# Kernel tuning notes

Hardware: AMD Instinct MI355X
Metric: run time of the kernel (lower is better)

Reference implementation:

```python
import jax, jax.numpy as jnp
from jax import lax
import numpy as np

WIN = 11
SIGMA = 1.5
PAD = WIN // 2
C1 = 0.01 ** 2
C2 = 0.03 ** 2


def _gauss1d():
    x = jnp.arange(WIN, dtype=jnp.float32) - (WIN // 2)
    k = jnp.exp(-(x ** 2) / (2.0 * SIGMA ** 2))
    return k / k.sum()


def _blur3d(x, k1d):
    # Separable 3D gaussian blur (mathematically identical to the outer-product
    # 3D kernel used by the torch module, since kernel3d = k1d (x) k1d (x) k1d).
    # x: [B, 1, D, H, W]
    dn = ('NCDHW', 'OIDHW', 'NCDHW')
    x = lax.conv_general_dilated(x, k1d.reshape(1, 1, WIN, 1, 1), (1, 1, 1),
                                 [(PAD, PAD), (0, 0), (0, 0)], dimension_numbers=dn)
    x = lax.conv_general_dilated(x, k1d.reshape(1, 1, 1, WIN, 1), (1, 1, 1),
                                 [(0, 0), (PAD, PAD), (0, 0)], dimension_numbers=dn)
    x = lax.conv_general_dilated(x, k1d.reshape(1, 1, 1, 1, WIN), (1, 1, 1),
                                 [(0, 0), (0, 0), (PAD, PAD)], dimension_numbers=dn)
    return x


def setup_inputs() -> dict:
    key = jax.random.key(0)
    k1, k2 = jax.random.split(key)
    shape = (2, 1, 192, 192, 192)
    img1 = jax.random.uniform(k1, shape, dtype=jnp.float32)
    img2 = jax.random.uniform(k2, shape, dtype=jnp.float32)
    return {"img1": img1, "img2": img2}


def reference(img1, img2):
    k1d = _gauss1d().astype(img1.dtype)
    mu1 = _blur3d(img1, k1d)
    mu2 = _blur3d(img2, k1d)
    mu1_sq = mu1 * mu1
    mu2_sq = mu2 * mu2
    mu1mu2 = mu1 * mu2
    sigma1 = _blur3d(img1 * img1, k1d) - mu1_sq
    sigma2 = _blur3d(img2 * img2, k1d) - mu2_sq
    sigma12 = _blur3d(img1 * img2, k1d) - mu1mu2
    num = (2.0 * mu1mu2 + C1) * (2.0 * sigma12 + C2)
    den = (mu1_sq + mu2_sq + C1) * (sigma1 + sigma2 + C2)
    ssim_map = num / den
    return ssim_map.mean()  # size_average=True
```

## Files before the change

kernel.cpp:

```cpp
#include <hip/hip_runtime.h>

#define NB 2
#define DD 192
#define HH 192
#define WW 192
#define HWSZ (HH * WW)
#define C1F 0.0001f
#define C2F 0.0009f

#define TH 16
#define TW 32
#define CHUNK 24
#define TSTEPS (CHUNK + 10)
#define NCH (DD / CHUNK)
#define NTH (HH / TH)
#define NTW (WW / TW)
#define NBLK (NB * NCH * NTH * NTW)

#define SROWS (TH + 10)
#define SCOLS 42
#define SQ 43
#define TQ 36
#define NSTG (SROWS * SCOLS)
#define NWT (SROWS * (TW / 4))

#define KWLIST { 0.00102838f, 0.00759876f, 0.03600077f, 0.10936071f, 0.21300556f, \
                 0.26601172f, 0.21300556f, 0.10936071f, 0.03600077f, 0.00759876f, 0.00102838f }

__device__ __forceinline__ float ssim_val(float mu1, float mu2, float A, float Bm) {
  const float mu1sq = mu1 * mu1, mu2sq = mu2 * mu2, mu12 = mu1 * mu2;
  const float num = (2.f * mu12 + C1F) * (0.5f * (A - Bm) - 2.f * mu12 + C2F);
  const float den = (mu1sq + mu2sq + C1F) * (0.5f * (A + Bm) - mu1sq - mu2sq + C2F);
  return num * __builtin_amdgcn_rcpf(den);
}

__global__ __launch_bounds__(256) void ssim_fused(
    const float* __restrict__ x, const float* __restrict__ y,
    float* __restrict__ partials) {
  const float KW[11] = KWLIST;

  int bid = blockIdx.x;
  const int tw = bid % NTW; bid /= NTW;
  const int th = bid % NTH; bid /= NTH;
  const int c  = bid % NCH; bid /= NCH;
  const int b  = bid;
  const int h0 = th * TH, w0 = tw * TW, c0 = c * CHUNK;

  __shared__ float4 s4[SROWS][SQ];
  __shared__ float4 t4[SROWS][TQ];

  const int tid = threadIdx.x;
  const int cl  = tid & 31;
  const int rg  = tid >> 5;
  const int r0  = 2 * rg;
  const int clp2 = (cl & ~3) | (((cl & 3) + (cl >> 2)) & 3);

  int  sIdx[5], sOff[5];
  bool sOk[5];
#pragma unroll
  for (int k = 0; k < 5; ++k) {
    const int q = tid + 256 * k;
    const bool act = (q < NSTG);
    const int row = q / SCOLS, col = q % SCOLS;
    const int gh = h0 - 5 + row, gw = w0 - 5 + col;
    sOk[k]  = act && (unsigned)gh < (unsigned)HH && (unsigned)gw < (unsigned)WW;
    sIdx[k] = row * SQ + col;
    sOff[k] = gh * WW + gw;
  }
  const bool wAct = (tid < NWT);
  const int  wr = tid >> 3;
  const int  wq = tid & 7;
  const int  tBase = wr * TQ + 4 * wq;
  const int  st0 = tBase + ((0 + wq) & 3);
  const int  st1 = tBase + ((1 + wq) & 3);
  const int  st2 = tBase + ((2 + wq) & 3);
  const int  st3 = tBase + ((3 + wq) & 3);

  {
    const float4 z = make_float4(0.f, 0.f, 0.f, 0.f);
    for (int q = tid; q < SROWS * SQ; q += 256) (&s4[0][0])[q] = z;
  }
  __syncthreads();

  const float* xb = x + (size_t)b * DD * HWSZ;
  const float* yb = y + (size_t)b * DD * HWSZ;

  float pend0[4][11], pend1[4][11];
#pragma unroll
  for (int f = 0; f < 4; ++f)
#pragma unroll
    for (int i = 0; i < 11; ++i) { pend0[f][i] = 0.f; pend1[f][i] = 0.f; }

  float px[5], py[5];
#pragma unroll
  for (int k = 0; k < 5; ++k) { px[k] = 0.f; py[k] = 0.f; }

  if (c0 >= 5) {
    const float* xs = xb + (size_t)(c0 - 5) * HWSZ;
    const float* ys = yb + (size_t)(c0 - 5) * HWSZ;
#pragma unroll
    for (int k = 0; k < 5; ++k)
      if (sOk[k]) { px[k] = xs[sOff[k]]; py[k] = ys[sOff[k]]; }
  }

  float lsum = 0.f;
  int p = 0;

  for (int t = 0; t < TSTEPS; ++t) {
    const int d = c0 - 5 + t;
    const bool dv = (d >= 0) && (d < DD);

    if (dv) {
#pragma unroll
      for (int k = 0; k < 5; ++k)
        if (sOk[k]) {
          const float xx = px[k], yy = py[k];
          const float sm = xx + yy, df = xx - yy;
          (&s4[0][0])[sIdx[k]] = make_float4(xx, yy, sm * sm, df * df);
        }
    }
    {
      const int dn = d + 1;
      if ((t + 1) < TSTEPS && dn >= 0 && dn < DD) {
        const float* xs = xb + (size_t)dn * HWSZ;
        const float* ys = yb + (size_t)dn * HWSZ;
#pragma unroll
        for (int k = 0; k < 5; ++k)
          if (sOk[k]) { px[k] = xs[sOff[k]]; py[k] = ys[sOff[k]]; }
      }
    }

    float4 B0 = make_float4(0.f, 0.f, 0.f, 0.f);
    float4 B1 = B0;

    if (dv) {
      __syncthreads();
      if (wAct) {
        const float4* srow = &s4[wr][0];
        float4 a0 = make_float4(0.f, 0.f, 0.f, 0.f), a1 = a0, a2 = a0, a3 = a0;
#pragma unroll
        for (int u = 0; u < 14; ++u) {
          const float4 v = srow[4 * wq + u];
          if (u <= 10)           { const float k = KW[u];     a0.x += k*v.x; a0.y += k*v.y; a0.z += k*v.z; a0.w += k*v.w; }
          if (u >= 1 && u <= 11) { const float k = KW[u - 1]; a1.x += k*v.x; a1.y += k*v.y; a1.z += k*v.z; a1.w += k*v.w; }
          if (u >= 2 && u <= 12) { const float k = KW[u - 2]; a2.x += k*v.x; a2.y += k*v.y; a2.z += k*v.z; a2.w += k*v.w; }
          if (u >= 3)            { const float k = KW[u - 3]; a3.x += k*v.x; a3.y += k*v.y; a3.z += k*v.z; a3.w += k*v.w; }
        }
        float4* tb = &t4[0][0];
        tb[st0] = a0; tb[st1] = a1; tb[st2] = a2; tb[st3] = a3;
      }
      __syncthreads();

#pragma unroll
      for (int u = 0; u < 12; ++u) {
        const float4 v = t4[r0 + u][clp2];
        if (u <= 10) { const float k = KW[u];     B0.x += k*v.x; B0.y += k*v.y; B0.z += k*v.z; B0.w += k*v.w; }
        if (u >= 1)  { const float k = KW[u - 1]; B1.x += k*v.x; B1.y += k*v.y; B1.z += k*v.z; B1.w += k*v.w; }
      }
    }

#define RING_CASE(P)                                                        \
    case P: {                                                               \
      if (dv) {                                                             \
        _Pragma("unroll")                                                   \
        for (int kk = 0; kk < 11; ++kk) {                                   \
          const int   sl = (P + 1 + kk) % 11;                               \
          const float wg = KW[kk];                                          \
          pend0[0][sl] += wg * B0.x; pend0[1][sl] += wg * B0.y;             \
          pend0[2][sl] += wg * B0.z; pend0[3][sl] += wg * B0.w;             \
          pend1[0][sl] += wg * B1.x; pend1[1][sl] += wg * B1.y;             \
          pend1[2][sl] += wg * B1.z; pend1[3][sl] += wg * B1.w;             \
        }                                                                   \
      }                                                                     \
      const int sc = (P + 1) % 11;                                          \
      if (t >= 10) {                                                        \
        lsum += ssim_val(pend0[0][sc], pend0[1][sc], pend0[2][sc], pend0[3][sc]); \
        lsum += ssim_val(pend1[0][sc], pend1[1][sc], pend1[2][sc], pend1[3][sc]); \
      }                                                                     \
      pend0[0][sc] = 0.f; pend0[1][sc] = 0.f;                               \
      pend0[2][sc] = 0.f; pend0[3][sc] = 0.f;                               \
      pend1[0][sc] = 0.f; pend1[1][sc] = 0.f;                               \
      pend1[2][sc] = 0.f; pend1[3][sc] = 0.f;                               \
    } break;

    switch (p) {
      RING_CASE(0) RING_CASE(1) RING_CASE(2) RING_CASE(3) RING_CASE(4)
      RING_CASE(5) RING_CASE(6) RING_CASE(7) RING_CASE(8) RING_CASE(9)
      RING_CASE(10)
    }
#undef RING_CASE
    p = (p + 1 == 11) ? 0 : p + 1;
  }

  for (int off = 32; off > 0; off >>= 1) lsum += __shfl_down(lsum, off, 64);
  __shared__ float wsum[4];
  if ((tid & 63) == 0) wsum[tid >> 6] = lsum;
  __syncthreads();
  if (tid == 0) partials[blockIdx.x] = wsum[0] + wsum[1] + wsum[2] + wsum[3];
}

__global__ __launch_bounds__(256) void ssim_reduce(
    const float* __restrict__ partials, float* __restrict__ out) {
  __shared__ double sd[256];
  double a = 0.0;
  for (int i = threadIdx.x; i < NBLK; i += 256) a += (double)partials[i];
  sd[threadIdx.x] = a;
  __syncthreads();
  for (int s = 128; s > 0; s >>= 1) {
    if ((int)threadIdx.x < s) sd[threadIdx.x] += sd[threadIdx.x + s];
    __syncthreads();
  }
  if (threadIdx.x == 0) {
    out[0] = (float)(sd[0] / (double)((size_t)NB * DD * HH * WW));
  }
}

extern "C" void kernel_launch(void* const* d_in, const int* in_sizes, int n_in,
                              void* d_out, int out_size, void* d_ws, size_t ws_size,
                              hipStream_t stream) {
  const float* img1 = (const float*)d_in[0];
  const float* img2 = (const float*)d_in[1];
  float* out = (float*)d_out;
  float* partials = (float*)d_ws;

  ssim_fused<<<NBLK, 256, 0, stream>>>(img1, img2, partials);
  ssim_reduce<<<1, 256, 0, stream>>>(partials, out);
}
```

Measured before the change: 167.1 us.

## Stage raw x,y pairs in LDS as float2 and enlarge depth chunk

```diff
diff --git a/kernel.cpp b/kernel.cpp
--- a/kernel.cpp
+++ b/kernel.cpp
@@ -10,7 +10,7 @@
 
 #define TH 16
 #define TW 32
-#define CHUNK 24
+#define CHUNK 32
 #define TSTEPS (CHUNK + 10)
 #define NCH (DD / CHUNK)
 #define NTH (HH / TH)
@@ -19,7 +19,7 @@
 
 #define SROWS (TH + 10)
 #define SCOLS 42
-#define SQ 43
+#define SP2 44
 #define TQ 36
 #define NSTG (SROWS * SCOLS)
 #define NWT (SROWS * (TW / 4))
@@ -46,7 +46,7 @@
   const int b  = bid;
   const int h0 = th * TH, w0 = tw * TW, c0 = c * CHUNK;
 
-  __shared__ float4 s4[SROWS][SQ];
+  __shared__ __align__(16) float2 s2[SROWS][SP2];
   __shared__ float4 t4[SROWS][TQ];
 
   const int tid = threadIdx.x;
@@ -64,7 +64,7 @@
     const int row = q / SCOLS, col = q % SCOLS;
     const int gh = h0 - 5 + row, gw = w0 - 5 + col;
     sOk[k]  = act && (unsigned)gh < (unsigned)HH && (unsigned)gw < (unsigned)WW;
-    sIdx[k] = row * SQ + col;
+    sIdx[k] = row * SP2 + col;
     sOff[k] = gh * WW + gw;
   }
   const bool wAct = (tid < NWT);
@@ -77,8 +77,8 @@
   const int  st3 = tBase + ((3 + wq) & 3);
 
   {
-    const float4 z = make_float4(0.f, 0.f, 0.f, 0.f);
-    for (int q = tid; q < SROWS * SQ; q += 256) (&s4[0][0])[q] = z;
+    const float2 z = make_float2(0.f, 0.f);
+    for (int q = tid; q < SROWS * SP2; q += 256) (&s2[0][0])[q] = z;
   }
   __syncthreads();
 
@@ -113,11 +113,7 @@
     if (dv) {
 #pragma unroll
       for (int k = 0; k < 5; ++k)
-        if (sOk[k]) {
-          const float xx = px[k], yy = py[k];
-          const float sm = xx + yy, df = xx - yy;
-          (&s4[0][0])[sIdx[k]] = make_float4(xx, yy, sm * sm, df * df);
-        }
+        if (sOk[k]) (&s2[0][0])[sIdx[k]] = make_float2(px[k], py[k]);
     }
     {
       const int dn = d + 1;
@@ -136,15 +132,23 @@
     if (dv) {
       __syncthreads();
       if (wAct) {
-        const float4* srow = &s4[wr][0];
+        const float4* srow4 = (const float4*)&s2[wr][0];
         float4 a0 = make_float4(0.f, 0.f, 0.f, 0.f), a1 = a0, a2 = a0, a3 = a0;
 #pragma unroll
-        for (int u = 0; u < 14; ++u) {
-          const float4 v = srow[4 * wq + u];
-          if (u <= 10)           { const float k = KW[u];     a0.x += k*v.x; a0.y += k*v.y; a0.z += k*v.z; a0.w += k*v.w; }
-          if (u >= 1 && u <= 11) { const float k = KW[u - 1]; a1.x += k*v.x; a1.y += k*v.y; a1.z += k*v.z; a1.w += k*v.w; }
-          if (u >= 2 && u <= 12) { const float k = KW[u - 2]; a2.x += k*v.x; a2.y += k*v.y; a2.z += k*v.z; a2.w += k*v.w; }
-          if (u >= 3)            { const float k = KW[u - 3]; a3.x += k*v.x; a3.y += k*v.y; a3.z += k*v.z; a3.w += k*v.w; }
+        for (int u2 = 0; u2 < 7; ++u2) {
+          const float4 v2 = srow4[2 * wq + u2];
+#pragma unroll
+          for (int h = 0; h < 2; ++h) {
+            const int   u  = 2 * u2 + h;
+            const float xx = h ? v2.z : v2.x;
+            const float yy = h ? v2.w : v2.y;
+            const float sm = xx + yy, df = xx - yy;
+            const float s2q = sm * sm, d2q = df * df;
+            if (u <= 10)           { const float k = KW[u];     a0.x += k*xx; a0.y += k*yy; a0.z += k*s2q; a0.w += k*d2q; }
+            if (u >= 1 && u <= 11) { const float k = KW[u - 1]; a1.x += k*xx; a1.y += k*yy; a1.z += k*s2q; a1.w += k*d2q; }
+            if (u >= 2 && u <= 12) { const float k = KW[u - 2]; a2.x += k*xx; a2.y += k*yy; a2.z += k*s2q; a2.w += k*d2q; }
+            if (u >= 3)            { const float k = KW[u - 3]; a3.x += k*xx; a3.y += k*yy; a3.z += k*s2q; a3.w += k*d2q; }
+          }
         }
         float4* tb = &t4[0][0];
         tb[st0] = a0; tb[st1] = a1; tb[st2] = a2; tb[st3] = a3;
```

Result: slower. 171.9 us (+2.8%).

## Split SSIM into 2D-blur pass writing fp16 intermediates and depth-blur pass

Applied to the files above, without the earlier changes.

```diff
diff --git a/kernel.cpp b/kernel.cpp
--- a/kernel.cpp
+++ b/kernel.cpp
@@ -1,22 +1,20 @@
 #include <hip/hip_runtime.h>
+#include <hip/hip_fp16.h>
 
 #define NB 2
 #define DD 192
 #define HH 192
 #define WW 192
 #define HWSZ (HH * WW)
+#define FELEMS ((size_t)NB * DD * HH * WW)
 #define C1F 0.0001f
 #define C2F 0.0009f
 
 #define TH 16
 #define TW 32
-#define CHUNK 24
-#define TSTEPS (CHUNK + 10)
-#define NCH (DD / CHUNK)
 #define NTH (HH / TH)
 #define NTW (WW / TW)
-#define NBLK (NB * NCH * NTH * NTW)
-
+#define NTILE (NTH * NTW)
 #define SROWS (TH + 10)
 #define SCOLS 42
 #define SQ 43
@@ -24,8 +22,21 @@
 #define NSTG (SROWS * SCOLS)
 #define NWT (SROWS * (TW / 4))
 
+#define FB_CHUNK 24
+#define FB_TSTEPS (FB_CHUNK + 10)
+#define FB_NCH (DD / FB_CHUNK)
+#define FB_NBLK (NB * FB_NCH * NTH * NTW)
+
+#define DC 48
+#define NDC (DD / DC)
+#define NP2 (NB * HH * NDC)
+
 #define KWLIST { 0.00102838f, 0.00759876f, 0.03600077f, 0.10936071f, 0.21300556f, \
                  0.26601172f, 0.21300556f, 0.10936071f, 0.03600077f, 0.00759876f, 0.00102838f }
+
+__device__ __forceinline__ void pk_fma(float2& acc, float2 a, float2 k2) {
+  asm("v_pk_fma_f32 %0, %1, %2, %0" : "+v"(acc) : "v"(a), "v"(k2));
+}
 
 __device__ __forceinline__ float ssim_val(float mu1, float mu2, float A, float Bm) {
   const float mu1sq = mu1 * mu1, mu2sq = mu2 * mu2, mu12 = mu1 * mu2;
@@ -34,7 +45,150 @@
   return num * __builtin_amdgcn_rcpf(den);
 }
 
-__global__ __launch_bounds__(256) void ssim_fused(
+__global__ __launch_bounds__(256) void ssim_p1(
+    const float* __restrict__ x, const float* __restrict__ y,
+    __half2* __restrict__ pa, __half2* __restrict__ pb) {
+  const float KW[11] = KWLIST;
+
+  int bid = blockIdx.x;
+  const int tile = bid % NTILE; bid /= NTILE;
+  const int d = bid % DD;
+  const int b = bid / DD;
+  const int tw = tile % NTW, th = tile / NTW;
+  const int h0 = th * TH, w0 = tw * TW;
+
+  __shared__ float4 s4[SROWS][SQ];
+  __shared__ float4 t4[SROWS][TQ];
+
+  const int tid = threadIdx.x;
+  const int cl = tid & 31;
+  const int r0 = 2 * (tid >> 5);
+  const int clp2 = (cl & ~3) | (((cl & 3) + (cl >> 2)) & 3);
+
+  const float* xs = x + (size_t)(b * DD + d) * HWSZ;
+  const float* ys = y + (size_t)(b * DD + d) * HWSZ;
+
+  for (int q = tid; q < NSTG; q += 256) {
+    const int row = q / SCOLS, col = q % SCOLS;
+    const int gh = h0 - 5 + row, gw = w0 - 5 + col;
+    float xx = 0.f, yy = 0.f;
+    if ((unsigned)gh < (unsigned)HH && (unsigned)gw < (unsigned)WW) {
+      const int o = gh * WW + gw;
+      xx = xs[o]; yy = ys[o];
+    }
+    const float sm = xx + yy, df = xx - yy;
+    s4[row][col] = make_float4(xx, yy, sm * sm, df * df);
+  }
+  __syncthreads();
+
+  if (tid < NWT) {
+    const int wr = tid >> 3, wq = tid & 7;
+    const float4* srow = &s4[wr][0];
+    float4 a0 = make_float4(0.f, 0.f, 0.f, 0.f), a1 = a0, a2 = a0, a3 = a0;
+#pragma unroll
+    for (int u = 0; u < 14; ++u) {
+      const float4 v = srow[4 * wq + u];
+      if (u <= 10)           { const float k = KW[u];     a0.x += k*v.x; a0.y += k*v.y; a0.z += k*v.z; a0.w += k*v.w; }
+      if (u >= 1 && u <= 11) { const float k = KW[u - 1]; a1.x += k*v.x; a1.y += k*v.y; a1.z += k*v.z; a1.w += k*v.w; }
+      if (u >= 2 && u <= 12) { const float k = KW[u - 2]; a2.x += k*v.x; a2.y += k*v.y; a2.z += k*v.z; a2.w += k*v.w; }
+      if (u >= 3)            { const float k = KW[u - 3]; a3.x += k*v.x; a3.y += k*v.y; a3.z += k*v.z; a3.w += k*v.w; }
+    }
+    float4* tb = &t4[0][0];
+    const int tBase = wr * TQ + 4 * wq;
+    tb[tBase + ((0 + wq) & 3)] = a0;
+    tb[tBase + ((1 + wq) & 3)] = a1;
+    tb[tBase + ((2 + wq) & 3)] = a2;
+    tb[tBase + ((3 + wq) & 3)] = a3;
+  }
+  __syncthreads();
+
+  float4 B0 = make_float4(0.f, 0.f, 0.f, 0.f), B1 = B0;
+#pragma unroll
+  for (int u = 0; u < 12; ++u) {
+    const float4 v = t4[r0 + u][clp2];
+    if (u <= 10) { const float k = KW[u];     B0.x += k*v.x; B0.y += k*v.y; B0.z += k*v.z; B0.w += k*v.w; }
+    if (u >= 1)  { const float k = KW[u - 1]; B1.x += k*v.x; B1.y += k*v.y; B1.z += k*v.z; B1.w += k*v.w; }
+  }
+  const size_t idx0 = ((size_t)(b * DD + d) * HH + (h0 + r0)) * WW + (w0 + cl);
+  pa[idx0] = __float22half2_rn(make_float2(B0.x, B0.y));
+  pb[idx0] = __float22half2_rn(make_float2(B0.z, B0.w));
+  const size_t idx1 = idx0 + WW;
+  pa[idx1] = __float22half2_rn(make_float2(B1.x, B1.y));
+  pb[idx1] = __float22half2_rn(make_float2(B1.z, B1.w));
+}
+
+__global__ __launch_bounds__(192) void ssim_p2(
+    const __half2* __restrict__ pa, const __half2* __restrict__ pb,
+    float* __restrict__ partials) {
+  const float KW[11] = KWLIST;
+  float2 KW2[11];
+#pragma unroll
+  for (int i = 0; i < 11; ++i) KW2[i] = make_float2(KW[i], KW[i]);
+
+  int bid = blockIdx.x;
+  const int h = bid % HH; bid /= HH;
+  const int dc = bid % NDC;
+  const int b = bid / NDC;
+  const int w = threadIdx.x;
+
+  const size_t rowoff = ((size_t)b * DD * HH + h) * WW + w;
+
+  float2 ra[11], rb[11];
+#pragma unroll
+  for (int i = 0; i < 11; ++i) { ra[i] = make_float2(0.f, 0.f); rb[i] = ra[i]; }
+
+  float lsum = 0.f;
+  const int dbase = dc * DC - 5;
+
+  __half2 va = __floats2half2_rn(0.f, 0.f), vb = va;
+  if (dbase >= 0) {
+    const size_t o = rowoff + (size_t)dbase * HWSZ;
+    va = pa[o]; vb = pb[o];
+  }
+
+  int p = 0;
+  for (int s = 0; s < DC + 10; ++s) {
+    const int d = dbase + s;
+    __half2 na = __floats2half2_rn(0.f, 0.f), nb2 = na;
+    const int dn = d + 1;
+    if ((s + 1) < DC + 10 && dn >= 0 && dn < DD) {
+      const size_t o = rowoff + (size_t)dn * HWSZ;
+      na = pa[o]; nb2 = pb[o];
+    }
+    const float2 fa = __half22float2(va);
+    const float2 fb = __half22float2(vb);
+
+#define RC2(P)                                                              \
+    case P: {                                                               \
+      _Pragma("unroll")                                                     \
+      for (int kk = 0; kk < 11; ++kk) {                                     \
+        const int sl = (P + 1 + kk) % 11;                                   \
+        pk_fma(ra[sl], fa, KW2[kk]);                                        \
+        pk_fma(rb[sl], fb, KW2[kk]);                                        \
+      }                                                                     \
+      const int sc = (P + 1) % 11;                                          \
+      if (s >= 10)                                                          \
+        lsum += ssim_val(ra[sc].x, ra[sc].y, rb[sc].x, rb[sc].y);           \
+      ra[sc] = make_float2(0.f, 0.f); rb[sc] = make_float2(0.f, 0.f);       \
+    } break;
+
+    switch (p) {
+      RC2(0) RC2(1) RC2(2) RC2(3) RC2(4) RC2(5)
+      RC2(6) RC2(7) RC2(8) RC2(9) RC2(10)
+    }
+#undef RC2
+    p = (p + 1 == 11) ? 0 : p + 1;
+    va = na; vb = nb2;
+  }
+
+  for (int off = 32; off > 0; off >>= 1) lsum += __shfl_down(lsum, off, 64);
+  __shared__ float wsum[3];
+  if ((threadIdx.x & 63) == 0) wsum[threadIdx.x >> 6] = lsum;
+  __syncthreads();
+  if (threadIdx.x == 0) partials[blockIdx.x] = wsum[0] + wsum[1] + wsum[2];
+}
+
+__global__ __launch_bounds__(256) void ssim_fb(
     const float* __restrict__ x, const float* __restrict__ y,
     float* __restrict__ partials) {
   const float KW[11] = KWLIST;
@@ -42,17 +196,16 @@
   int bid = blockIdx.x;
   const int tw = bid % NTW; bid /= NTW;
   const int th = bid % NTH; bid /= NTH;
-  const int c  = bid % NCH; bid /= NCH;
+  const int c  = bid % FB_NCH; bid /= FB_NCH;
   const int b  = bid;
-  const int h0 = th * TH, w0 = tw * TW, c0 = c * CHUNK;
+  const int h0 = th * TH, w0 = tw * TW, c0 = c * FB_CHUNK;
 
   __shared__ float4 s4[SROWS][SQ];
   __shared__ float4 t4[SROWS][TQ];
 
   const int tid = threadIdx.x;
   const int cl  = tid & 31;
-  const int rg  = tid >> 5;
-  const int r0  = 2 * rg;
+  const int r0  = 2 * (tid >> 5);
   const int clp2 = (cl & ~3) | (((cl & 3) + (cl >> 2)) & 3);
 
   int  sIdx[5], sOff[5];
@@ -106,7 +259,7 @@
   float lsum = 0.f;
   int p = 0;
 
-  for (int t = 0; t < TSTEPS; ++t) {
+  for (int t = 0; t < FB_TSTEPS; ++t) {
     const int d = c0 - 5 + t;
     const bool dv = (d >= 0) && (d < DD);
 
@@ -121,7 +274,7 @@
     }
     {
       const int dn = d + 1;
-      if ((t + 1) < TSTEPS && dn >= 0 && dn < DD) {
+      if ((t + 1) < FB_TSTEPS && dn >= 0 && dn < DD) {
         const float* xs = xb + (size_t)dn * HWSZ;
         const float* ys = yb + (size_t)dn * HWSZ;
 #pragma unroll
@@ -200,19 +353,17 @@
 }
 
 __global__ __launch_bounds__(256) void ssim_reduce(
-    const float* __restrict__ partials, float* __restrict__ out) {
+    const float* __restrict__ partials, int n, float* __restrict__ out) {
   __shared__ double sd[256];
   double a = 0.0;
-  for (int i = threadIdx.x; i < NBLK; i += 256) a += (double)partials[i];
+  for (int i = threadIdx.x; i < n; i += 256) a += (double)partials[i];
   sd[threadIdx.x] = a;
   __syncthreads();
   for (int s = 128; s > 0; s >>= 1) {
     if ((int)threadIdx.x < s) sd[threadIdx.x] += sd[threadIdx.x + s];
     __syncthreads();
   }
-  if (threadIdx.x == 0) {
-    out[0] = (float)(sd[0] / (double)((size_t)NB * DD * HH * WW));
-  }
+  if (threadIdx.x == 0) out[0] = (float)(sd[0] / (double)FELEMS);
 }
 
 extern "C" void kernel_launch(void* const* d_in, const int* in_sizes, int n_in,
@@ -221,8 +372,18 @@
   const float* img1 = (const float*)d_in[0];
   const float* img2 = (const float*)d_in[1];
   float* out = (float*)d_out;
-  float* partials = (float*)d_ws;
-
-  ssim_fused<<<NBLK, 256, 0, stream>>>(img1, img2, partials);
-  ssim_reduce<<<1, 256, 0, stream>>>(partials, out);
-}
+
+  const size_t need = FELEMS * 8 + (size_t)NP2 * 4 + 256;
+  if (ws_size >= need) {
+    __half2* pa = (__half2*)d_ws;
+    __half2* pb = pa + FELEMS;
+    float* partials = (float*)(pb + FELEMS);
+    ssim_p1<<<NB * DD * NTILE, 256, 0, stream>>>(img1, img2, pa, pb);
+    ssim_p2<<<NP2, 192, 0, stream>>>(pa, pb, partials);
+    ssim_reduce<<<1, 256, 0, stream>>>(partials, NP2, out);
+  } else {
+    float* partials = (float*)d_ws;
+    ssim_fb<<<FB_NBLK, 256, 0, stream>>>(img1, img2, partials);
+    ssim_reduce<<<1, 256, 0, stream>>>(partials, FB_NBLK, out);
+  }
+}
```

After: 187.9 us. +12.4%, slower.
